# Optimization experiments

Measured on AMD Instinct MI355X. Metric: run time of the kernel, lower is better.

## Reference

```python
import jax, jax.numpy as jnp
import numpy as np

B, S, H, I, E, TOPK, KS = 4, 4096, 1024, 512, 16, 2, 3


def setup_inputs() -> dict:
    key = jax.random.key(0)
    ks = jax.random.split(key, 9)
    sc = 0.02
    return {
        "hidden_states": jax.random.normal(ks[0], (B, S, H), dtype=jnp.float32),
        "router_w": jax.random.normal(ks[1], (H, E), dtype=jnp.float32) * sc,
        "router_bias": jnp.zeros((E,), dtype=jnp.float32),
        "expert_gate_w": jax.random.normal(ks[2], (E - 1, H, I), dtype=jnp.float32) * sc,
        "expert_up_w": jax.random.normal(ks[3], (E - 1, H, I), dtype=jnp.float32) * sc,
        "expert_down_w": jax.random.normal(ks[4], (E - 1, I, H), dtype=jnp.float32) * sc,
        "conv_w": jax.random.normal(ks[5], (I, H, KS), dtype=jnp.float32) * sc,
        "shared_up_w": jax.random.normal(ks[6], (H, I), dtype=jnp.float32) * sc,
        "shared_down_w": jax.random.normal(ks[7], (I, H), dtype=jnp.float32) * sc,
    }


def reference(hidden_states, router_w, router_bias, expert_gate_w, expert_up_w,
              expert_down_w, conv_w, shared_up_w, shared_down_w):
    b, s, h = hidden_states.shape
    flat = hidden_states.reshape(b * s, h)  # (T, H)

    # ---- Router (mlp type, temperature=1, no noise at eval) ----
    logits = (flat @ router_w).astype(jnp.float32) + router_bias  # (T, E)
    probs = jax.nn.softmax(logits, axis=-1)
    top_w, top_i = jax.lax.top_k(probs, TOPK)  # (T, K)
    norm_w = top_w / (jnp.sum(top_w, axis=-1, keepdims=True) + 1e-6)
    norm_w = norm_w.astype(hidden_states.dtype)
    # Dense combine weights (T, E): scatter top-k weights into expert slots
    combine = jnp.sum(jax.nn.one_hot(top_i, E, dtype=norm_w.dtype) * norm_w[..., None], axis=1)

    # ---- Routed experts: E-1 SwiGLU MLPs + 1 Identity (index E-1) ----
    routed = combine[:, E - 1:E] * flat  # identity expert contribution
    for e in range(E - 1):
        y = (jax.nn.silu(flat @ expert_gate_w[e]) * (flat @ expert_up_w[e])) @ expert_down_w[e]
        routed = routed + combine[:, e:e + 1] * y
    routed = routed.reshape(b, s, h)

    # ---- Shared expert: causal conv1d gate * up, then down ----
    x_ncw = jnp.transpose(hidden_states, (0, 2, 1))  # (B, H, S)
    gate = jax.lax.conv_general_dilated(
        x_ncw, conv_w, window_strides=(1,), padding=[(KS - 1, 0)],
        dimension_numbers=("NCW", "OIW", "NCW"))  # (B, I, S)
    gate = jnp.transpose(gate, (0, 2, 1))  # (B, S, I)
    shared = (jax.nn.silu(gate) * (hidden_states @ shared_up_w)) @ shared_down_w

    return shared + routed
```

## Files before the change

kernel.cpp:

```cpp
#include <hip/hip_runtime.h>

typedef unsigned short u16;
typedef __attribute__((ext_vector_type(4))) float f32x4;
using bf16x8 = __attribute__((ext_vector_type(8))) short;
typedef __attribute__((ext_vector_type(8))) unsigned short u16x8;
typedef __attribute__((ext_vector_type(4))) unsigned short u16x4;

#define GAS __attribute__((address_space(1)))
#define LAS __attribute__((address_space(3)))

__device__ __forceinline__ float bf2f(u16 u) {
  unsigned v = ((unsigned)u) << 16;
  float f;
  __builtin_memcpy(&f, &v, 4);
  return f;
}
__device__ __forceinline__ u16 f2bf(float f) {
  unsigned u;
  __builtin_memcpy(&u, &f, 4);
  u += 0x7fffu + ((u >> 16) & 1u);
  return (u16)(u >> 16);
}
__device__ __forceinline__ void llds16(const void* g, void* l) {
  __builtin_amdgcn_global_load_lds((const GAS unsigned*)g, (LAS unsigned*)l, 16, 0, 0);
}

__global__ void cvtx_k(const float* __restrict__ x, u16* __restrict__ xb) {
  const long i = (long)blockIdx.x * 256 + threadIdx.x;
  f32x4 v = *(const f32x4*)(x + i * 4);
  u16x4 r;
#pragma unroll
  for (int j = 0; j < 4; ++j) r[j] = f2bf(v[j]);
  *(u16x4*)(xb + i * 4) = r;
}

__global__ __launch_bounds__(256) void router_k(const float* __restrict__ x,
    const float* __restrict__ rw, const float* __restrict__ rb,
    int* __restrict__ topk_idx, float* __restrict__ topk_w, int* __restrict__ ib) {
  __shared__ float xs[4][32 * 65];
  __shared__ float wsm[4][32 * 16];
  __shared__ float part[4][64 * 17];
  __shared__ int cnt[16];
  const int tid = threadIdx.x;
  const int wv = __builtin_amdgcn_readfirstlane(tid >> 6);
  const int lane = tid & 63;
  const int tok0 = blockIdx.x * 64;
  const int rr = lane >> 3;
  const int c4 = (lane & 7) * 4;

  float acc[16];
#pragma unroll
  for (int e = 0; e < 16; ++e) acc[e] = 0.f;

  for (int c = 0; c < 8; ++c) {
    const int hb = wv * 256 + c * 32;
    {
      f32x4 wa = *(const f32x4*)(rw + hb * 16 + lane * 4);
      f32x4 wb = *(const f32x4*)(rw + hb * 16 + 256 + lane * 4);
      *(f32x4*)&wsm[wv][lane * 4] = wa;
      *(f32x4*)&wsm[wv][256 + lane * 4] = wb;
    }
#pragma unroll
    for (int i = 0; i < 8; ++i) {
      const int row = i * 8 + rr;
      f32x4 v = *(const f32x4*)(x + (long)(tok0 + row) * 1024 + hb + c4);
#pragma unroll
      for (int j = 0; j < 4; ++j) xs[wv][(c4 + j) * 65 + row] = v[j];
    }
    __syncthreads();
#pragma unroll
    for (int h = 0; h < 32; ++h) {
      const float xv = xs[wv][h * 65 + lane];
      const float* wrow = &wsm[wv][h * 16];
#pragma unroll
      for (int q = 0; q < 4; ++q) {
        f32x4 w4 = *(const f32x4*)(wrow + q * 4);
#pragma unroll
        for (int e = 0; e < 4; ++e) acc[q * 4 + e] += xv * w4[e];
      }
    }
    __syncthreads();
  }
#pragma unroll
  for (int e = 0; e < 16; ++e) part[wv][lane * 17 + e] = acc[e];
  if (tid < 16) cnt[tid] = 0;
  __syncthreads();
  if (tid < 64) {
    float p[16];
#pragma unroll
    for (int e = 0; e < 16; ++e)
      p[e] = part[0][tid * 17 + e] + part[1][tid * 17 + e] +
             part[2][tid * 17 + e] + part[3][tid * 17 + e] + rb[e];
    float mx = p[0];
#pragma unroll
    for (int e = 1; e < 16; ++e) mx = fmaxf(mx, p[e]);
    float sum = 0.f;
#pragma unroll
    for (int e = 0; e < 16; ++e) { p[e] = __expf(p[e] - mx); sum += p[e]; }
    int i0 = 0; float p0 = p[0];
    for (int e = 1; e < 16; ++e) if (p[e] > p0) { p0 = p[e]; i0 = e; }
    int i1 = -1; float p1 = -1.f;
    for (int e = 0; e < 16; ++e) if (e != i0 && p[e] > p1) { p1 = p[e]; i1 = e; }
    const float inv = 1.f / sum;
    p0 *= inv; p1 *= inv;
    const float d = p0 + p1 + 1e-6f;
    const int t = tok0 + tid;
    topk_idx[t * 2] = i0; topk_idx[t * 2 + 1] = i1;
    topk_w[t * 2] = p0 / d;
    topk_w[t * 2 + 1] = p1 / d;
    if (i0 < 15) atomicAdd(&cnt[i0], 1);
    if (i1 < 15) atomicAdd(&cnt[i1], 1);
  }
  __syncthreads();
  if (tid < 15 && cnt[tid] > 0) atomicAdd(&ib[tid], cnt[tid]);
}

__global__ void zero_k(int* __restrict__ ib) {
  if (threadIdx.x < 16) ib[threadIdx.x] = 0;
}

__global__ void scan_k(int* __restrict__ ib) {
  if (threadIdx.x != 0 || blockIdx.x != 0) return;
  int off = 0;
  for (int ee = 0; ee < 15; ++ee) { ib[16 + ee] = off; ib[32 + ee] = off; off += ib[ee]; }
  ib[16 + 15] = off;
  int nm = 0;
  for (int ee = 0; ee < 15; ++ee) {
    const int st = ib[16 + ee], en = ib[16 + ee + 1];
    for (int r = st; r < en; r += 128) {
      ib[64 + nm * 4] = ee; ib[64 + nm * 4 + 1] = r; ib[64 + nm * 4 + 2] = en; ++nm;
    }
  }
  ib[48] = nm;
}

__global__ __launch_bounds__(256) void scatter_k(const int* __restrict__ topk_idx,
                          const float* __restrict__ topk_w,
                          int* __restrict__ ib, int* __restrict__ tok_ids,
                          float* __restrict__ tok_w, int* __restrict__ slot_map) {
  __shared__ int cnt[16], base[16];
  const int tid = threadIdx.x;
  const int j = blockIdx.x * 256 + tid;
  if (tid < 16) cnt[tid] = 0;
  __syncthreads();
  const int e = topk_idx[j];
  int lo = 0;
  if (e < 15) lo = atomicAdd(&cnt[e], 1);
  __syncthreads();
  if (tid < 15 && cnt[tid] > 0) base[tid] = atomicAdd(&ib[32 + tid], cnt[tid]);
  __syncthreads();
  if (e < 15) {
    const int pos = base[e] + lo;
    tok_ids[pos] = j >> 1;
    tok_w[pos] = topk_w[j];
    slot_map[j] = pos;
  } else {
    slot_map[j] = -1;
  }
}

__global__ void transpose_k(const float* __restrict__ src, u16* __restrict__ dst, int R, int C) {
  __shared__ float tile[32][33];
  src += (long)blockIdx.z * R * C;
  dst += (long)blockIdx.z * R * C;
  const int c0 = blockIdx.x * 32, r0 = blockIdx.y * 32;
  const int tx = threadIdx.x & 31, ty = threadIdx.x >> 5;
#pragma unroll
  for (int i = ty; i < 32; i += 8) tile[i][tx] = src[(long)(r0 + i) * C + c0 + tx];
  __syncthreads();
#pragma unroll
  for (int i = ty; i < 32; i += 8) dst[(long)(c0 + i) * R + r0 + tx] = f2bf(tile[tx][i]);
}

__global__ void convt_k(const float* __restrict__ cw, u16* __restrict__ dst) {
  const int idx = blockIdx.x * 256 + threadIdx.x;
  if (idx >= 3 * 512 * 1024) return;
  const int k = idx >> 19;
  const int rem = idx & 524287;
  const int i = rem >> 10, h = rem & 1023;
  dst[idx] = f2bf(cw[i * 3072 + h * 3 + k]);
}

template<int V>
__global__ __launch_bounds__(256, 2)
void gemm_k(const u16* __restrict__ Abase, const u16* __restrict__ Bt0,
            const u16* __restrict__ Bt1, void* __restrict__ OUTv,
            const int* __restrict__ tbl, const int* __restrict__ nmt,
            const int* __restrict__ tok_ids, const float* __restrict__ tok_w,
            int K, int ldA, int ldOut) {
  __shared__ u16 lds[16384];
  u16* OUT = (u16*)OUTv;
  float* OUTF = (float*)OUTv;
  const int tid = threadIdx.x;
  const int wave = tid >> 6, lane = tid & 63;
  const int quad = lane >> 4, l16 = lane & 15;
  const int rA = tid >> 2;
  const int sub8 = (tid & 3) * 8;
  const int sub8s = ((tid & 3) ^ ((tid >> 3) & 3)) * 8;

  int e = 0, row0, row_end;
  if constexpr (V <= 1) {
    const int mt = blockIdx.x;
    if (mt >= *nmt) return;
    e = tbl[mt * 4]; row0 = tbl[mt * 4 + 1]; row_end = tbl[mt * 4 + 2];
  } else {
    row0 = blockIdx.x * 128; row_end = row0 + 128;
  }
  const int n0 = blockIdx.y * ((V == 0) ? 64 : 128);

  f32x4 acc[2][8];
#pragma unroll
  for (int i = 0; i < 2; ++i)
#pragma unroll
    for (int j = 0; j < 8; ++j) acc[i][j] = (f32x4){0.f, 0.f, 0.f, 0.f};

  const int swz8 = (((l16 >> 1) & 3) ^ quad) * 8;
  const int aoff0 = (wave * 32 + l16) * 32 + swz8;
  const int aoff1 = aoff0 + 512;

  int cur = 0;
  u16x8 va0n, va1n;

  const int nph = (V == 3) ? 3 : 1;
  const int kIters = K / 32;
  for (int ph = 0; ph < nph; ++ph) {
    const u16 *pA0, *pA1, *pB0, *pB1;
    bool zero0 = false;
    if constexpr (V == 0) {
      const int t0i = tok_ids[min(row0 + rA, row_end - 1)];
      const int t1i = tok_ids[min(row0 + rA + 64, row_end - 1)];
      pA0 = Abase + (long)t0i * 1024 + sub8s;
      pA1 = Abase + (long)t1i * 1024 + sub8s;
      pB0 = Bt0 + ((long)e * 512 + n0 + rA) * 1024 + sub8s;
      pB1 = Bt1 + ((long)e * 512 + n0 + rA) * 1024 + sub8s;
    } else if constexpr (V == 1) {
      pA0 = Abase + (long)min(row0 + rA, row_end - 1) * 512 + sub8s;
      pA1 = Abase + (long)min(row0 + rA + 64, row_end - 1) * 512 + sub8s;
      pB0 = Bt0 + ((long)e * 1024 + n0 + rA) * 512 + sub8s;
      pB1 = Bt0 + ((long)e * 1024 + n0 + rA + 64) * 512 + sub8s;
    } else if constexpr (V == 2 || V == 4) {
      pA0 = Abase + (long)(row0 + rA) * ldA + sub8s;
      pA1 = Abase + (long)(row0 + rA + 64) * ldA + sub8s;
      pB0 = Bt0 + (long)(n0 + rA) * K + sub8s;
      pB1 = Bt0 + (long)(n0 + rA + 64) * K + sub8s;
    } else {
      const int bb = row0 >> 12, s0 = row0 & 4095;
      const int si0 = s0 + ph - 2 + rA;
      zero0 = si0 < 0;
      pA0 = Abase + ((long)bb * 4096 + (si0 < 0 ? 0 : si0)) * 1024 + sub8s;
      pA1 = Abase + ((long)bb * 4096 + (si0 + 64)) * 1024 + sub8s;
      pB0 = Bt0 + (long)ph * 512 * 1024 + (long)(n0 + rA) * 1024 + sub8s;
      pB1 = Bt0 + (long)ph * 512 * 1024 + (long)(n0 + rA + 64) * 1024 + sub8s;
    }

    if constexpr (V == 3) {
      va0n = *(const u16x8*)pA0; pA0 += 32;
      va1n = *(const u16x8*)pA1; pA1 += 32;
      if (zero0) va0n = (u16x8){0, 0, 0, 0, 0, 0, 0, 0};
      *(u16x8*)&lds[cur + rA * 32 + sub8] = va0n;
      *(u16x8*)&lds[cur + (rA + 64) * 32 + sub8] = va1n;
    } else {
      llds16(pA0, &lds[cur + wave * 512]); pA0 += 32;
      llds16(pA1, &lds[cur + 2048 + wave * 512]); pA1 += 32;
    }
    llds16(pB0, &lds[cur + 4096 + wave * 512]); pB0 += 32;
    llds16(pB1, &lds[cur + 6144 + wave * 512]); pB1 += 32;
    __syncthreads();

    for (int kb = 0; kb < kIters; ++kb) {
      const int nxt = cur ^ 8192;
      const bool pre = (kb + 1 < kIters);
      if constexpr (V == 3) {
        if (pre) {
          llds16(pB0, &lds[nxt + 4096 + wave * 512]); pB0 += 32;
          llds16(pB1, &lds[nxt + 6144 + wave * 512]); pB1 += 32;
          va0n = *(const u16x8*)pA0; pA0 += 32;
          va1n = *(const u16x8*)pA1; pA1 += 32;
          if (zero0) va0n = (u16x8){0, 0, 0, 0, 0, 0, 0, 0};
        }
      } else {
        if (pre) {
          llds16(pA0, &lds[nxt + wave * 512]); pA0 += 32;
          llds16(pA1, &lds[nxt + 2048 + wave * 512]); pA1 += 32;
          llds16(pB0, &lds[nxt + 4096 + wave * 512]); pB0 += 32;
          llds16(pB1, &lds[nxt + 6144 + wave * 512]); pB1 += 32;
        }
      }
      bf16x8 a0 = *(const bf16x8*)&lds[cur + aoff0];
      bf16x8 a1 = *(const bf16x8*)&lds[cur + aoff1];
#pragma unroll
      for (int nt = 0; nt < 8; ++nt) {
        bf16x8 b = *(const bf16x8*)&lds[cur + 4096 + (nt * 16 + l16) * 32 + swz8];
        acc[0][nt] = __builtin_amdgcn_mfma_f32_16x16x32_bf16(a0, b, acc[0][nt], 0, 0, 0);
        acc[1][nt] = __builtin_amdgcn_mfma_f32_16x16x32_bf16(a1, b, acc[1][nt], 0, 0, 0);
      }
      if constexpr (V == 3) {
        if (pre) {
          *(u16x8*)&lds[nxt + rA * 32 + sub8] = va0n;
          *(u16x8*)&lds[nxt + (rA + 64) * 32 + sub8] = va1n;
        }
      }
      __syncthreads();
      cur = nxt;
    }
  }

  const int rbase = wave * 32;
  if constexpr (V == 0) {
#pragma unroll
    for (int mt = 0; mt < 2; ++mt)
#pragma unroll
      for (int r = 0; r < 4; ++r) {
        const int row = rbase + mt * 16 + quad * 4 + r;
#pragma unroll
        for (int nt = 0; nt < 4; ++nt) {
          float g = acc[mt][nt][r], u = acc[mt][nt + 4][r];
          float sg = g / (1.f + __expf(-g));
          lds[row * 64 + nt * 16 + l16] = f2bf(sg * u);
        }
      }
    __syncthreads();
#pragma unroll
    for (int i = 0; i < 4; ++i) {
      const int c = i * 256 + tid;
      const int row = c >> 3, s8 = (c & 7) * 8;
      const int slot = row0 + row;
      if (slot < row_end)
        *(u16x8*)(OUT + (long)slot * ldOut + n0 + s8) = *(const u16x8*)&lds[row * 64 + s8];
    }
  } else if constexpr (V == 1) {
#pragma unroll
    for (int mt = 0; mt < 2; ++mt)
#pragma unroll
      for (int r = 0; r < 4; ++r) {
        const int row = rbase + mt * 16 + quad * 4 + r;
        const float wgt = tok_w[min(row0 + row, row_end - 1)];
#pragma unroll
        for (int nt = 0; nt < 8; ++nt)
          lds[row * 128 + nt * 16 + l16] = f2bf(acc[mt][nt][r] * wgt);
      }
    __syncthreads();
#pragma unroll
    for (int i = 0; i < 8; ++i) {
      const int c = i * 256 + tid;
      const int row = c >> 4, s8 = (c & 15) * 8;
      const int slot = row0 + row;
      if (slot < row_end)
        *(u16x8*)(OUT + (long)slot * ldOut + n0 + s8) = *(const u16x8*)&lds[row * 128 + s8];
    }
  } else if constexpr (V == 2) {
#pragma unroll
    for (int mt = 0; mt < 2; ++mt)
#pragma unroll
      for (int r = 0; r < 4; ++r) {
        const int row = rbase + mt * 16 + quad * 4 + r;
#pragma unroll
        for (int nt = 0; nt < 8; ++nt)
          lds[row * 128 + nt * 16 + l16] = f2bf(acc[mt][nt][r]);
      }
    __syncthreads();
#pragma unroll
    for (int i = 0; i < 8; ++i) {
      const int c = i * 256 + tid;
      const int row = c >> 4, s8 = (c & 15) * 8;
      *(u16x8*)(OUT + (long)(row0 + row) * ldOut + n0 + s8) = *(const u16x8*)&lds[row * 128 + s8];
    }
  } else if constexpr (V == 3) {
#pragma unroll
    for (int mt = 0; mt < 2; ++mt)
#pragma unroll
      for (int r = 0; r < 4; ++r) {
        const int row = rbase + mt * 16 + quad * 4 + r;
#pragma unroll
        for (int nt = 0; nt < 8; ++nt) {
          float g = acc[mt][nt][r];
          lds[row * 128 + nt * 16 + l16] = f2bf(g / (1.f + __expf(-g)));
        }
      }
    __syncthreads();
#pragma unroll
    for (int i = 0; i < 8; ++i) {
      const int c = i * 256 + tid;
      const int row = c >> 4, s8 = (c & 15) * 8;
      const long o = (long)(row0 + row) * ldOut + n0 + s8;
      u16x8 sg8 = *(const u16x8*)&lds[row * 128 + s8];
      u16x8 up8 = *(const u16x8*)(OUT + o);
      u16x8 res;
#pragma unroll
      for (int j = 0; j < 8; ++j) res[j] = f2bf(bf2f(sg8[j]) * bf2f(up8[j]));
      *(u16x8*)(OUT + o) = res;
    }
  } else {
#pragma unroll
    for (int mt = 0; mt < 2; ++mt)
#pragma unroll
      for (int r = 0; r < 4; ++r) {
        const int row = row0 + rbase + mt * 16 + quad * 4 + r;
#pragma unroll
        for (int nt = 0; nt < 8; ++nt)
          OUTF[(long)row * ldOut + n0 + nt * 16 + l16] = acc[mt][nt][r];
      }
  }
}

__global__ void final_k(const float* __restrict__ x, const u16* __restrict__ Y,
                        const int* __restrict__ slot_map, const float* __restrict__ topk_w,
                        float* __restrict__ out) {
  const long idx = (long)blockIdx.x * 256 + threadIdx.x;
  const int t = (int)(idx >> 8), cc = ((int)idx & 255) * 4;
  const long ob = (long)t * 1024 + cc;
  f32x4 o = *(const f32x4*)(out + ob);
#pragma unroll
  for (int k2 = 0; k2 < 2; ++k2) {
    const int sm = slot_map[t * 2 + k2];
    if (sm >= 0) {
      u16x4 y = *(const u16x4*)(Y + (long)sm * 1024 + cc);
#pragma unroll
      for (int j = 0; j < 4; ++j) o[j] += bf2f(y[j]);
    } else {
      const float w = topk_w[t * 2 + k2];
      f32x4 xv = *(const f32x4*)(x + ob);
#pragma unroll
      for (int j = 0; j < 4; ++j) o[j] += w * xv[j];
    }
  }
  *(f32x4*)(out + ob) = o;
}

extern "C" void kernel_launch(void* const* d_in, const int* in_sizes, int n_in,
                              void* d_out, int out_size, void* d_ws, size_t ws_size,
                              hipStream_t stream) {
  (void)in_sizes; (void)n_in; (void)out_size; (void)ws_size;
  const float* x   = (const float*)d_in[0];
  const float* rw  = (const float*)d_in[1];
  const float* rb  = (const float*)d_in[2];
  const float* gw  = (const float*)d_in[3];
  const float* uw  = (const float*)d_in[4];
  const float* dw  = (const float*)d_in[5];
  const float* cw  = (const float*)d_in[6];
  const float* suw = (const float*)d_in[7];
  const float* sdw = (const float*)d_in[8];
  float* out = (float*)d_out;

  char* base = (char*)d_ws;
  size_t off = 0;
  auto alloc = [&](size_t b) { void* p = base + off; off = (off + b + 255) & ~(size_t)255; return p; };
  u16* xb     = (u16*)alloc(16777216ull * 2);
  u16* gate_t = (u16*)alloc(15ull * 512 * 1024 * 2);
  u16* up_t   = (u16*)alloc(15ull * 512 * 1024 * 2);
  u16* down_t = (u16*)alloc(15ull * 1024 * 512 * 2);
  u16* conv_t = (u16*)alloc(3ull * 512 * 1024 * 2);
  u16* sup_t  = (u16*)alloc(512ull * 1024 * 2);
  u16* sdn_t  = (u16*)alloc(512ull * 1024 * 2);
  u16* inter  = (u16*)alloc(32768ull * 512 * 2);
  u16* Y      = (u16*)alloc(32768ull * 1024 * 2);
  u16* UP     = (u16*)alloc(16384ull * 512 * 2);
  int*   topi    = (int*)alloc(32768 * 4);
  float* topw    = (float*)alloc(32768 * 4);
  int*   smap    = (int*)alloc(32768 * 4);
  int*   tok_ids = (int*)alloc(32768 * 4);
  float* tokw    = (float*)alloc(32768 * 4);
  int*   ib      = (int*)alloc(8192);

  zero_k<<<1, 64, 0, stream>>>(ib);
  cvtx_k<<<16384, 256, 0, stream>>>(x, xb);
  transpose_k<<<dim3(16, 32, 15), 256, 0, stream>>>(gw, gate_t, 1024, 512);
  transpose_k<<<dim3(16, 32, 15), 256, 0, stream>>>(uw, up_t, 1024, 512);
  transpose_k<<<dim3(32, 16, 15), 256, 0, stream>>>(dw, down_t, 512, 1024);
  transpose_k<<<dim3(16, 32, 1), 256, 0, stream>>>(suw, sup_t, 1024, 512);
  transpose_k<<<dim3(32, 16, 1), 256, 0, stream>>>(sdw, sdn_t, 512, 1024);
  convt_k<<<6144, 256, 0, stream>>>(cw, conv_t);
  router_k<<<256, 256, 0, stream>>>(x, rw, rb, topi, topw, ib);
  scan_k<<<1, 64, 0, stream>>>(ib);
  scatter_k<<<128, 256, 0, stream>>>(topi, topw, ib, tok_ids, tokw, smap);
  gemm_k<0><<<dim3(272, 8), 256, 0, stream>>>(xb, gate_t, up_t, inter, ib + 64, ib + 48,
                                              tok_ids, tokw, 1024, 1024, 512);
  gemm_k<1><<<dim3(272, 8), 256, 0, stream>>>(inter, down_t, nullptr, Y, ib + 64, ib + 48,
                                              nullptr, tokw, 512, 512, 1024);
  gemm_k<2><<<dim3(128, 4), 256, 0, stream>>>(xb, sup_t, nullptr, UP, nullptr, nullptr,
                                              nullptr, nullptr, 1024, 1024, 512);
  gemm_k<3><<<dim3(128, 4), 256, 0, stream>>>(xb, conv_t, nullptr, UP, nullptr, nullptr,
                                              nullptr, nullptr, 1024, 1024, 512);
  gemm_k<4><<<dim3(128, 8), 256, 0, stream>>>(UP, sdn_t, nullptr, out, nullptr, nullptr,
                                              nullptr, nullptr, 512, 512, 1024);
  final_k<<<16384, 256, 0, stream>>>(x, Y, smap, topw, out);
}
```

Before: 603.2 us.

## Triple-buffer LDS staging with vmcnt waits in non-conv GEMM variants

For the expert and dense GEMM variants, replaces the double-buffered global-to-LDS pipeline with a three-stage ring buffer. It waits on vmcnt counters rather than a full __syncthreads, and raises wave priority around the MFMA block. The intent is to keep two tiles in flight so global load latency is hidden better. The cost is that LDS per block grows from 32KB to 48KB, which may limit occupancy. The conv variant keeps its original double-buffered path.

```diff
diff --git a/kernel.cpp b/kernel.cpp
--- a/kernel.cpp
+++ b/kernel.cpp
@@ -188,7 +188,7 @@
             const int* __restrict__ tbl, const int* __restrict__ nmt,
             const int* __restrict__ tok_ids, const float* __restrict__ tok_w,
             int K, int ldA, int ldOut) {
-  __shared__ u16 lds[16384];
+  __shared__ u16 lds[24576];
   u16* OUT = (u16*)OUTv;
   float* OUTF = (float*)OUTv;
   const int tid = threadIdx.x;
@@ -217,15 +217,10 @@
   const int swz8 = (((l16 >> 1) & 3) ^ quad) * 8;
   const int aoff0 = (wave * 32 + l16) * 32 + swz8;
   const int aoff1 = aoff0 + 512;
-
-  int cur = 0;
-  u16x8 va0n, va1n;
-
-  const int nph = (V == 3) ? 3 : 1;
   const int kIters = K / 32;
-  for (int ph = 0; ph < nph; ++ph) {
+
+  if constexpr (V != 3) {
     const u16 *pA0, *pA1, *pB0, *pB1;
-    bool zero0 = false;
     if constexpr (V == 0) {
       const int t0i = tok_ids[min(row0 + rA, row_end - 1)];
       const int t1i = tok_ids[min(row0 + rA + 64, row_end - 1)];
@@ -238,39 +233,70 @@
       pA1 = Abase + (long)min(row0 + rA + 64, row_end - 1) * 512 + sub8s;
       pB0 = Bt0 + ((long)e * 1024 + n0 + rA) * 512 + sub8s;
       pB1 = Bt0 + ((long)e * 1024 + n0 + rA + 64) * 512 + sub8s;
-    } else if constexpr (V == 2 || V == 4) {
+    } else {
       pA0 = Abase + (long)(row0 + rA) * ldA + sub8s;
       pA1 = Abase + (long)(row0 + rA + 64) * ldA + sub8s;
       pB0 = Bt0 + (long)(n0 + rA) * K + sub8s;
       pB1 = Bt0 + (long)(n0 + rA + 64) * K + sub8s;
-    } else {
+    }
+    auto STAGE = [&](int buf) {
+      llds16(pA0, &lds[buf + wave * 512]); pA0 += 32;
+      llds16(pA1, &lds[buf + 2048 + wave * 512]); pA1 += 32;
+      llds16(pB0, &lds[buf + 4096 + wave * 512]); pB0 += 32;
+      llds16(pB1, &lds[buf + 6144 + wave * 512]); pB1 += 32;
+    };
+    STAGE(0);
+    STAGE(8192);
+    int cur = 0, stg = 16384;
+    for (int kb = 0; kb < kIters; ++kb) {
+      if (kb + 1 < kIters) {
+        asm volatile("s_waitcnt vmcnt(4)" ::: "memory");
+      } else {
+        asm volatile("s_waitcnt vmcnt(0)" ::: "memory");
+      }
+      __builtin_amdgcn_s_barrier();
+      if (kb + 2 < kIters) {
+        STAGE(stg);
+        stg = (stg == 16384) ? 0 : stg + 8192;
+      }
+      bf16x8 a0 = *(const bf16x8*)&lds[cur + aoff0];
+      bf16x8 a1 = *(const bf16x8*)&lds[cur + aoff1];
+      __builtin_amdgcn_s_setprio(1);
+#pragma unroll
+      for (int nt = 0; nt < 8; ++nt) {
+        bf16x8 b = *(const bf16x8*)&lds[cur + 4096 + (nt * 16 + l16) * 32 + swz8];
+        acc[0][nt] = __builtin_amdgcn_mfma_f32_16x16x32_bf16(a0, b, acc[0][nt], 0, 0, 0);
+        acc[1][nt] = __builtin_amdgcn_mfma_f32_16x16x32_bf16(a1, b, acc[1][nt], 0, 0, 0);
+      }
+      __builtin_amdgcn_s_setprio(0);
+      cur = (cur == 16384) ? 0 : cur + 8192;
+    }
+    __builtin_amdgcn_s_barrier();
+  } else {
+    int cur = 0;
+    u16x8 va0n, va1n;
+    for (int ph = 0; ph < 3; ++ph) {
+      const u16 *pA0, *pA1, *pB0, *pB1;
       const int bb = row0 >> 12, s0 = row0 & 4095;
       const int si0 = s0 + ph - 2 + rA;
-      zero0 = si0 < 0;
+      const bool zero0 = si0 < 0;
       pA0 = Abase + ((long)bb * 4096 + (si0 < 0 ? 0 : si0)) * 1024 + sub8s;
       pA1 = Abase + ((long)bb * 4096 + (si0 + 64)) * 1024 + sub8s;
       pB0 = Bt0 + (long)ph * 512 * 1024 + (long)(n0 + rA) * 1024 + sub8s;
       pB1 = Bt0 + (long)ph * 512 * 1024 + (long)(n0 + rA + 64) * 1024 + sub8s;
-    }
-
-    if constexpr (V == 3) {
+
       va0n = *(const u16x8*)pA0; pA0 += 32;
       va1n = *(const u16x8*)pA1; pA1 += 32;
       if (zero0) va0n = (u16x8){0, 0, 0, 0, 0, 0, 0, 0};
       *(u16x8*)&lds[cur + rA * 32 + sub8] = va0n;
       *(u16x8*)&lds[cur + (rA + 64) * 32 + sub8] = va1n;
-    } else {
-      llds16(pA0, &lds[cur + wave * 512]); pA0 += 32;
-      llds16(pA1, &lds[cur + 2048 + wave * 512]); pA1 += 32;
-    }
-    llds16(pB0, &lds[cur + 4096 + wave * 512]); pB0 += 32;
-    llds16(pB1, &lds[cur + 6144 + wave * 512]); pB1 += 32;
-    __syncthreads();
-
-    for (int kb = 0; kb < kIters; ++kb) {
-      const int nxt = cur ^ 8192;
-      const bool pre = (kb + 1 < kIters);
-      if constexpr (V == 3) {
+      llds16(pB0, &lds[cur + 4096 + wave * 512]); pB0 += 32;
+      llds16(pB1, &lds[cur + 6144 + wave * 512]); pB1 += 32;
+      __syncthreads();
+
+      for (int kb = 0; kb < kIters; ++kb) {
+        const int nxt = cur ^ 8192;
+        const bool pre = (kb + 1 < kIters);
         if (pre) {
           llds16(pB0, &lds[nxt + 4096 + wave * 512]); pB0 += 32;
           llds16(pB1, &lds[nxt + 6144 + wave * 512]); pB1 += 32;
@@ -278,30 +304,21 @@
           va1n = *(const u16x8*)pA1; pA1 += 32;
           if (zero0) va0n = (u16x8){0, 0, 0, 0, 0, 0, 0, 0};
         }
-      } else {
-        if (pre) {
-          llds16(pA0, &lds[nxt + wave * 512]); pA0 += 32;
-          llds16(pA1, &lds[nxt + 2048 + wave * 512]); pA1 += 32;
-          llds16(pB0, &lds[nxt + 4096 + wave * 512]); pB0 += 32;
-          llds16(pB1, &lds[nxt + 6144 + wave * 512]); pB1 += 32;
+        bf16x8 a0 = *(const bf16x8*)&lds[cur + aoff0];
+        bf16x8 a1 = *(const bf16x8*)&lds[cur + aoff1];
+#pragma unroll
+        for (int nt = 0; nt < 8; ++nt) {
+          bf16x8 b = *(const bf16x8*)&lds[cur + 4096 + (nt * 16 + l16) * 32 + swz8];
+          acc[0][nt] = __builtin_amdgcn_mfma_f32_16x16x32_bf16(a0, b, acc[0][nt], 0, 0, 0);
+          acc[1][nt] = __builtin_amdgcn_mfma_f32_16x16x32_bf16(a1, b, acc[1][nt], 0, 0, 0);
         }
-      }
-      bf16x8 a0 = *(const bf16x8*)&lds[cur + aoff0];
-      bf16x8 a1 = *(const bf16x8*)&lds[cur + aoff1];
-#pragma unroll
-      for (int nt = 0; nt < 8; ++nt) {
-        bf16x8 b = *(const bf16x8*)&lds[cur + 4096 + (nt * 16 + l16) * 32 + swz8];
-        acc[0][nt] = __builtin_amdgcn_mfma_f32_16x16x32_bf16(a0, b, acc[0][nt], 0, 0, 0);
-        acc[1][nt] = __builtin_amdgcn_mfma_f32_16x16x32_bf16(a1, b, acc[1][nt], 0, 0, 0);
-      }
-      if constexpr (V == 3) {
         if (pre) {
           *(u16x8*)&lds[nxt + rA * 32 + sub8] = va0n;
           *(u16x8*)&lds[nxt + (rA + 64) * 32 + sub8] = va1n;
         }
-      }
-      __syncthreads();
-      cur = nxt;
+        __syncthreads();
+        cur = nxt;
+      }
     }
   }
 
```

Measured after the change: 611.9 us. About the same (+1.4%).
